# Optimization experiments

Measured on AMD Instinct MI355X. Metric: run time of the kernel, lower is better.

Reference implementation:

```python
import jax, jax.numpy as jnp
import numpy as np

EPS = 1e-6

def setup_inputs() -> dict:
    key = jax.random.key(0)
    k1, k2, k3 = jax.random.split(key, 3)
    D = 1024
    return {
        "x": jax.random.normal(k1, (2, 2048, D), dtype=jnp.float32),
        "w_norm": jnp.ones((D,), dtype=jnp.float32),
        "w_qkv": jax.random.normal(k2, (3 * D, D), dtype=jnp.float32) * (1.0 / np.sqrt(D)),
        "w_out": jax.random.normal(k3, (D, D), dtype=jnp.float32) * (1.0 / np.sqrt(D)),
        "window_size": 128,
        "n_heads": 16,
    }

def reference(x, w_norm, w_qkv, w_out, window_size, n_heads):
    B, L, D = x.shape
    H = n_heads
    dh = D // H
    skip = x
    # RMSNorm
    rms = jnp.sqrt(jnp.mean(x * x, axis=-1, keepdims=True) + EPS)
    xn = w_norm * (x / rms)
    # QKV projection (torch Linear: y = x @ W.T)
    qkv = xn @ w_qkv.T  # [B, L, 3D]
    q, k, v = jnp.split(qkv, 3, axis=-1)
    q = q.reshape(B, L, H, dh).transpose(0, 2, 1, 3)  # [B,H,L,dh]
    k = k.reshape(B, L, H, dh).transpose(0, 2, 1, 3)
    v = v.reshape(B, L, H, dh).transpose(0, 2, 1, 3)
    scores = jnp.einsum("bhid,bhjd->bhij", q, k) / np.sqrt(dh)  # [B,H,L,L]
    # Symmetric window: token i attends to j in [i - w//2, i + w//2]
    idx = jnp.arange(L)
    half = window_size // 2
    band = jnp.abs(idx[:, None] - idx[None, :]) <= half  # [L, L]
    scores = jnp.where(band, scores, -jnp.inf)
    attn = jax.nn.softmax(scores, axis=-1)  # zeros outside band, matches torch loop
    out = jnp.einsum("bhij,bhjd->bhid", attn, v)  # [B,H,L,dh]
    out = out.transpose(0, 2, 1, 3).reshape(B, L, D)
    out = out @ w_out.T
    return out + skip
```

## Files before the change

### kernel.cpp

```cpp
#include <hip/hip_runtime.h>
#include <hip/hip_bf16.h>
#include <cstdint>

typedef float f32x4 __attribute__((ext_vector_type(4)));
typedef float f32x16 __attribute__((ext_vector_type(16)));
typedef short s16x8 __attribute__((ext_vector_type(8)));
typedef short s16x4 __attribute__((ext_vector_type(4)));
typedef unsigned int u32x2 __attribute__((ext_vector_type(2)));
typedef unsigned int u32x4 __attribute__((ext_vector_type(4)));

constexpr int B_ = 2, L_ = 2048, D_ = 1024, H_ = 16, DH = 64, HALF = 64;
constexpr int M_ROWS = B_ * L_;
constexpr int QKV_N = 3 * D_;

__device__ __forceinline__ void gload16(const void* g, void* l) {
    __builtin_amdgcn_global_load_lds(
        (const __attribute__((address_space(1))) unsigned int*)g,
        (__attribute__((address_space(3))) unsigned int*)l, 16, 0, 0);
}

__device__ __forceinline__ void cfence() {
    __builtin_amdgcn_sched_barrier(0);
    asm volatile("" ::: "memory");
}

__global__ __launch_bounds__(256) void prep_kernel(const float* __restrict__ x,
                                                   const float* __restrict__ wn,
                                                   const float* __restrict__ wq,
                                                   const float* __restrict__ wo,
                                                   __hip_bfloat16* __restrict__ xn,
                                                   __hip_bfloat16* __restrict__ oq,
                                                   __hip_bfloat16* __restrict__ oo) {
    constexpr int NQ4 = QKV_N * D_ / 4;
    constexpr int NCVT = NQ4 + D_ * D_ / 4;
    constexpr int CVTBLK = NCVT / 256;
    int bid = blockIdx.x;
    if (bid < CVTBLK) {
        int i = bid * 256 + threadIdx.x;
        const float* src; __hip_bfloat16* dst; int j;
        if (i < NQ4) { src = wq; dst = oq; j = i; }
        else         { src = wo; dst = oo; j = i - NQ4; }
        float4 v = reinterpret_cast<const float4*>(src)[j];
        s16x4 pk;
        float vals[4] = {v.x, v.y, v.z, v.w};
#pragma unroll
        for (int e = 0; e < 4; ++e) {
            __hip_bfloat16 t = __float2bfloat16(vals[e]);
            pk[e] = *reinterpret_cast<short*>(&t);
        }
        *(s16x4*)(dst + (size_t)j * 4) = pk;
    } else {
        int w = threadIdx.x >> 6, lane = threadIdx.x & 63;
        int row = (bid - CVTBLK) * 4 + w;
        const float4* xr = reinterpret_cast<const float4*>(x + (size_t)row * D_);
        const float4* wr = reinterpret_cast<const float4*>(wn);
        float4 v[4];
        float ss = 0.f;
#pragma unroll
        for (int c = 0; c < 4; ++c) {
            v[c] = xr[c * 64 + lane];
            ss += v[c].x * v[c].x + v[c].y * v[c].y + v[c].z * v[c].z + v[c].w * v[c].w;
        }
#pragma unroll
        for (int off = 32; off; off >>= 1) ss += __shfl_xor(ss, off);
        float rinv = rsqrtf(ss * (1.0f / D_) + 1e-6f);
#pragma unroll
        for (int c = 0; c < 4; ++c) {
            float4 wv = wr[c * 64 + lane];
            s16x4 pk;
            float vals[4] = {v[c].x * rinv * wv.x, v[c].y * rinv * wv.y,
                             v[c].z * rinv * wv.z, v[c].w * rinv * wv.w};
#pragma unroll
            for (int e = 0; e < 4; ++e) {
                __hip_bfloat16 t = __float2bfloat16(vals[e]);
                pk[e] = *reinterpret_cast<short*>(&t);
            }
            *(s16x4*)(xn + (size_t)row * D_ + (c * 64 + lane) * 4) = pk;
        }
    }
}

__global__ __launch_bounds__(512, 2) void gemm_qkv_kernel(const __hip_bfloat16* __restrict__ A,
                                                          const __hip_bfloat16* __restrict__ Bt,
                                                          __hip_bfloat16* __restrict__ Cbf,
                                                          __hip_bfloat16* __restrict__ vT,
                                                          int M, int N, int K) {
    constexpr int ATILE = 16384;
    constexpr int BUFB = 32768;
    __shared__ __align__(16) char smem[4 * BUFB];

    const int tid = threadIdx.x;
    const int lane = tid & 63;
    const int wid = tid >> 6;

    int nwg = gridDim.x * gridDim.y;
    int lin = blockIdx.y * gridDim.x + blockIdx.x;
    int cpx = nwg >> 3;
    int swz = (lin & 7) * cpx + (lin >> 3);
    int bx = swz % gridDim.x;
    int by = swz / gridDim.x;

    const int rowBase = by * 256;
    const int colBase = bx * 256;
    const int NT = K >> 5;

    const int r0 = tid >> 2;
    const int cA = ((tid & 3) ^ ((r0 ^ (r0 >> 2)) & 3)) << 3;
    const __hip_bfloat16* aG = A + (size_t)(rowBase + r0) * K + cA;
    const __hip_bfloat16* bG = Bt + (size_t)(colBase + r0) * K + cA;
    const int dstW = wid << 10;

    const int wm = wid >> 2, wn = wid & 3;
    const int l15 = lane & 15, hi = lane >> 4;
    const int swzl = (l15 ^ (l15 >> 2)) & 3;
    const int aRd = wm * 8192 + l15 * 64 + ((hi ^ swzl) << 4);
    const int bRd = ATILE + wn * 4096 + l15 * 64 + ((hi ^ swzl) << 4);

    f32x4 acc[8][4];
#pragma unroll
    for (int m = 0; m < 8; ++m)
#pragma unroll
        for (int n = 0; n < 4; ++n) acc[m][n] = (f32x4){0.f, 0.f, 0.f, 0.f};

    auto STAGE = [&](int tt) {
        char* base = smem + (tt & 3) * BUFB + dstW;
        const __hip_bfloat16* as = aG + (size_t)tt * 32;
        const __hip_bfloat16* bs = bG + (size_t)tt * 32;
        gload16(as, base);
        gload16(as + (size_t)128 * K, base + 8192);
        gload16(bs, base + ATILE);
        gload16(bs + (size_t)128 * K, base + ATILE + 8192);
    };

    STAGE(0);
    STAGE(1);

    for (int t = 0; t < NT; ++t) {
        if (t + 2 < NT) {
            STAGE(t + 2);
            asm volatile("s_waitcnt vmcnt(8)" ::: "memory");
        } else if (t + 1 < NT) {
            asm volatile("s_waitcnt vmcnt(4)" ::: "memory");
        } else {
            asm volatile("s_waitcnt vmcnt(0)" ::: "memory");
        }
        asm volatile("s_waitcnt lgkmcnt(0)" ::: "memory");
        __builtin_amdgcn_s_barrier();
        cfence();

        const char* tb = smem + (t & 3) * BUFB;
        s16x8 af[8], bf[4];
#pragma unroll
        for (int mf = 0; mf < 8; ++mf)
            af[mf] = *(const s16x8*)(tb + aRd + mf * 1024);
#pragma unroll
        for (int nf = 0; nf < 4; ++nf)
            bf[nf] = *(const s16x8*)(tb + bRd + nf * 1024);

        __builtin_amdgcn_s_setprio(1);
#pragma unroll
        for (int mf = 0; mf < 8; ++mf)
#pragma unroll
            for (int nf = 0; nf < 4; ++nf)
                acc[mf][nf] = __builtin_amdgcn_mfma_f32_16x16x32_bf16(af[mf], bf[nf],
                                                                      acc[mf][nf], 0, 0, 0);
        __builtin_amdgcn_s_setprio(0);
    }

    if (colBase < 2 * D_) {
#pragma unroll
        for (int mf = 0; mf < 8; ++mf)
#pragma unroll
            for (int nf = 0; nf < 4; ++nf) {
                int col = colBase + wn * 64 + nf * 16 + l15;
                int row0 = rowBase + wm * 128 + mf * 16 + 4 * hi;
#pragma unroll
                for (int r = 0; r < 4; ++r)
                    Cbf[(size_t)(row0 + r) * N + col] = __float2bfloat16(acc[mf][nf][r]);
            }
    } else {
        int bb2 = rowBase >> 11, i0 = rowBase & (L_ - 1);
#pragma unroll
        for (int p = 0; p < 2; ++p) {
            if (p) __syncthreads();
            if ((wn >> 1) == p) {
#pragma unroll
                for (int mf = 0; mf < 8; ++mf)
#pragma unroll
                    for (int nf = 0; nf < 4; ++nf) {
                        int clp = (wn & 1) * 64 + nf * 16 + l15;
#pragma unroll
                        for (int r = 0; r < 4; ++r) {
                            int rl = wm * 128 + mf * 16 + 4 * hi + r;
                            __hip_bfloat16 t = __float2bfloat16(acc[mf][nf][r]);
                            *(short*)(smem + clp * 528 + rl * 2) = *reinterpret_cast<short*>(&t);
                        }
                    }
            }
            __syncthreads();
            {
                int c = tid >> 2, qd = tid & 3;
                int gcol = colBase + p * 128 + c - 2 * D_;
                int hh = gcol >> 6, dd = gcol & 63;
                __hip_bfloat16* dstp = vT + ((size_t)(bb2 * H_ + hh) * DH + dd) * L_ + i0 + qd * 64;
#pragma unroll
                for (int ch = 0; ch < 8; ++ch)
                    *(s16x8*)(dstp + ch * 8) = *(const s16x8*)(smem + c * 528 + qd * 128 + ch * 16);
            }
        }
    }
}

__global__ __launch_bounds__(256, 3) void gemm_proj_kernel(const __hip_bfloat16* __restrict__ A,
                                                           const __hip_bfloat16* __restrict__ Bt,
                                                           float* __restrict__ Cf,
                                                           const float* __restrict__ resid,
                                                           int M, int N, int K) {
    constexpr int BM = 128, BN = 64;
    constexpr int ATILE = BM * 64;
    constexpr int BTILE = BN * 64;
    constexpr int BUFB = ATILE + BTILE;
    __shared__ __align__(16) char smem[4 * BUFB];

    const int tid = threadIdx.x;
    const int lane = tid & 63;
    const int wid = tid >> 6;

    int nwg = gridDim.x * gridDim.y;
    int lin = blockIdx.y * gridDim.x + blockIdx.x;
    int cpx = nwg >> 3;
    int swz = (lin & 7) * cpx + (lin >> 3);
    int bx = swz % gridDim.x;
    int by = swz / gridDim.x;

    const int rowBase = by * BM;
    const int colBase = bx * BN;
    const int NT = K >> 5;

    const int r0 = tid >> 2;
    const int cS = ((tid & 3) ^ ((r0 ^ (r0 >> 2)) & 3)) << 3;
    const __hip_bfloat16* aG = A + (size_t)(rowBase + r0) * K + cS;
    const __hip_bfloat16* bG = Bt + (size_t)(colBase + r0) * K + cS;
    const int dstW = wid << 10;

    const int wm = wid >> 1, wn = wid & 1;
    const int l15 = lane & 15, hi = lane >> 4;
    const int swzl = (l15 ^ (l15 >> 2)) & 3;
    const int aRd = wm * 4096 + l15 * 64 + ((hi ^ swzl) << 4);
    const int bRd = ATILE + wn * 2048 + l15 * 64 + ((hi ^ swzl) << 4);

    f32x4 acc[4][2];
#pragma unroll
    for (int m = 0; m < 4; ++m)
#pragma unroll
        for (int n = 0; n < 2; ++n) acc[m][n] = (f32x4){0.f, 0.f, 0.f, 0.f};

    auto STAGE = [&](int tt) {
        char* base = smem + (tt & 3) * BUFB + dstW;
        const __hip_bfloat16* as = aG + (size_t)tt * 32;
        const __hip_bfloat16* bs = bG + (size_t)tt * 32;
        gload16(as, base);
        gload16(as + (size_t)64 * K, base + 4096);
        gload16(bs, base + ATILE);
    };

    STAGE(0);
    STAGE(1);

    for (int t = 0; t < NT; ++t) {
        if (t + 2 < NT) {
            STAGE(t + 2);
            asm volatile("s_waitcnt vmcnt(6)" ::: "memory");
        } else if (t + 1 < NT) {
            asm volatile("s_waitcnt vmcnt(3)" ::: "memory");
        } else {
            asm volatile("s_waitcnt vmcnt(0)" ::: "memory");
        }
        asm volatile("s_waitcnt lgkmcnt(0)" ::: "memory");
        __builtin_amdgcn_s_barrier();
        cfence();

        const char* tb = smem + (t & 3) * BUFB;
        s16x8 af[4], bf[2];
#pragma unroll
        for (int mf = 0; mf < 4; ++mf)
            af[mf] = *(const s16x8*)(tb + aRd + mf * 1024);
#pragma unroll
        for (int nf = 0; nf < 2; ++nf)
            bf[nf] = *(const s16x8*)(tb + bRd + nf * 1024);

        __builtin_amdgcn_s_setprio(1);
#pragma unroll
        for (int mf = 0; mf < 4; ++mf)
#pragma unroll
            for (int nf = 0; nf < 2; ++nf)
                acc[mf][nf] = __builtin_amdgcn_mfma_f32_16x16x32_bf16(af[mf], bf[nf],
                                                                      acc[mf][nf], 0, 0, 0);
        __builtin_amdgcn_s_setprio(0);
    }

#pragma unroll
    for (int mf = 0; mf < 4; ++mf)
#pragma unroll
        for (int nf = 0; nf < 2; ++nf) {
            int col = colBase + wn * 32 + nf * 16 + l15;
            int row0 = rowBase + wm * 64 + mf * 16 + 4 * hi;
#pragma unroll
            for (int r = 0; r < 4; ++r)
                Cf[(size_t)(row0 + r) * N + col] = acc[mf][nf][r] + resid[(size_t)(row0 + r) * N + col];
        }
}

__global__ __launch_bounds__(128, 2) void attn_mfma_kernel(const __hip_bfloat16* __restrict__ qkv,
                                                           const __hip_bfloat16* __restrict__ vT,
                                                           __hip_bfloat16* __restrict__ attn) {
    int tid = threadIdx.x;
    int w = tid >> 6;
    int lane = tid & 63;
    int l31 = lane & 31, hi1 = lane >> 5;
    int tq = blockIdx.x, h = blockIdx.y, b = blockIdx.z;
    int qbase = tq * 64 + 32 * w;
    int kb = qbase - HALF;
    int qg = qbase + l31;
    const __hip_bfloat16* qkvb = qkv + (size_t)(b * L_) * QKV_N;
    const __hip_bfloat16* vTg = vT + (size_t)(b * H_ + h) * DH * L_;

    s16x8 qf[4];
#pragma unroll
    for (int kk = 0; kk < 4; ++kk)
        qf[kk] = *(const s16x8*)(qkvb + (size_t)qg * QKV_N + h * DH + kk * 16 + hi1 * 8);

    f32x16 T[5];
#pragma unroll
    for (int kt = 0; kt < 5; ++kt) T[kt] = (f32x16)(0.f);
#pragma unroll
    for (int kt = 0; kt < 5; ++kt) {
        int keyg = kb + 32 * kt + l31;
        int kc = keyg < 0 ? 0 : (keyg > L_ - 1 ? L_ - 1 : keyg);
        const __hip_bfloat16* kp = qkvb + (size_t)kc * QKV_N + D_ + h * DH + hi1 * 8;
#pragma unroll
        for (int kk = 0; kk < 4; ++kk) {
            s16x8 kf = *(const s16x8*)(kp + kk * 16);
            T[kt] = __builtin_amdgcn_mfma_f32_32x32x16_bf16(kf, qf[kk], T[kt], 0, 0, 0);
        }
    }

    float mx = -1e30f;
#pragma unroll
    for (int kt = 0; kt < 5; ++kt) {
#pragma unroll
        for (int r = 0; r < 16; ++r) {
            int koff = (r & 3) + 8 * (r >> 2) + 4 * hi1;
            int keyg = kb + 32 * kt + koff;
            int del = keyg - qg;
            bool ok = (del >= -HALF) && (del <= HALF) && (keyg >= 0) && (keyg < L_);
            float t = ok ? T[kt][r] * 0.125f : -1e30f;
            T[kt][r] = t;
            mx = fmaxf(mx, t);
        }
    }
    mx = fmaxf(mx, __shfl_xor(mx, 32));
    float sum = 0.f;
#pragma unroll
    for (int kt = 0; kt < 5; ++kt) {
#pragma unroll
        for (int r = 0; r < 16; ++r) {
            float p = __expf(T[kt][r] - mx);
            T[kt][r] = p;
            sum += p;
        }
    }
    sum += __shfl_xor(sum, 32);
    float inv = 1.0f / sum;

    u32x4 pu[10];
#pragma unroll
    for (int kt = 0; kt < 5; ++kt) {
#pragma unroll
        for (int s = 0; s < 2; ++s) {
            unsigned P0, P1, P2, P3;
            asm("v_cvt_pk_bf16_f32 %0, %1, %2" : "=v"(P0) : "v"(T[kt][8 * s + 0]), "v"(T[kt][8 * s + 1]));
            asm("v_cvt_pk_bf16_f32 %0, %1, %2" : "=v"(P1) : "v"(T[kt][8 * s + 2]), "v"(T[kt][8 * s + 3]));
            asm("v_cvt_pk_bf16_f32 %0, %1, %2" : "=v"(P2) : "v"(T[kt][8 * s + 4]), "v"(T[kt][8 * s + 5]));
            asm("v_cvt_pk_bf16_f32 %0, %1, %2" : "=v"(P3) : "v"(T[kt][8 * s + 6]), "v"(T[kt][8 * s + 7]));
            u32x2 sA = __builtin_amdgcn_permlane32_swap(P0, P2, false, false);
            u32x2 sB = __builtin_amdgcn_permlane32_swap(P1, P3, false, false);
            pu[2 * kt + s] = (u32x4){sA[0], sB[0], sA[1], sB[1]};
        }
    }

    f32x16 O[2];
#pragma unroll
    for (int dt = 0; dt < 2; ++dt) O[dt] = (f32x16)(0.f);
#pragma unroll
    for (int t = 0; t < 10; ++t) {
        int kv = kb + 16 * t + 8 * hi1;
        kv = kv < 0 ? 0 : (kv > L_ - 8 ? L_ - 8 : kv);
        s16x8 pf = __builtin_bit_cast(s16x8, pu[t]);
#pragma unroll
        for (int dt = 0; dt < 2; ++dt) {
            s16x8 vf = *(const s16x8*)(vTg + (size_t)(32 * dt + l31) * L_ + kv);
            O[dt] = __builtin_amdgcn_mfma_f32_32x32x16_bf16(vf, pf, O[dt], 0, 0, 0);
        }
    }

    __hip_bfloat16* ob = attn + (size_t)(b * L_ + qg) * D_ + h * DH;
#pragma unroll
    for (int dt = 0; dt < 2; ++dt) {
#pragma unroll
        for (int rr = 0; rr < 4; ++rr) {
            s16x4 pk4;
#pragma unroll
            for (int j = 0; j < 4; ++j) {
                __hip_bfloat16 tb = __float2bfloat16(O[dt][4 * rr + j] * inv);
                pk4[j] = *reinterpret_cast<short*>(&tb);
            }
            *(s16x4*)(ob + 32 * dt + 8 * rr + 4 * hi1) = pk4;
        }
    }
}

extern "C" void kernel_launch(void* const* d_in, const int* in_sizes, int n_in,
                              void* d_out, int out_size, void* d_ws, size_t ws_size,
                              hipStream_t stream) {
    const float* x      = (const float*)d_in[0];
    const float* w_norm = (const float*)d_in[1];
    const float* w_qkv  = (const float*)d_in[2];
    const float* w_out  = (const float*)d_in[3];

    char* ws = (char*)d_ws;
    __hip_bfloat16* xn   = (__hip_bfloat16*)(ws);
    __hip_bfloat16* wq   = (__hip_bfloat16*)(ws + (8u  << 20));
    __hip_bfloat16* wo   = (__hip_bfloat16*)(ws + (14u << 20));
    __hip_bfloat16* qkv  = (__hip_bfloat16*)(ws + (16u << 20));
    __hip_bfloat16* attn = (__hip_bfloat16*)(ws + (40u << 20));
    __hip_bfloat16* vT   = (__hip_bfloat16*)(ws + (48u << 20));
    float* out = (float*)d_out;

    prep_kernel<<<4096 + M_ROWS / 4, 256, 0, stream>>>(x, w_norm, w_qkv, w_out, xn, wq, wo);

    gemm_qkv_kernel<<<dim3(QKV_N / 256, M_ROWS / 256), 512, 0, stream>>>(
        xn, wq, qkv, vT, M_ROWS, QKV_N, D_);

    attn_mfma_kernel<<<dim3(L_ / 64, H_, B_), 128, 0, stream>>>(qkv, vT, attn);

    gemm_proj_kernel<<<dim3(D_ / 64, M_ROWS / 128), 256, 0, stream>>>(
        attn, wo, out, x, M_ROWS, D_, D_);
}
```

Measured before the change: 89.91 us.

## Deepen QKV GEMM pipeline with register double-buffered A fragments

Restructures the QKV GEMM main loop to prefetch three stages ahead and to load the next tile's A fragments into a second register set while the current MFMAs run. The loop is unrolled by two so the register buffers swap without copies, and NT is made a compile-time constant. The V-transpose epilogue gains a barrier before reusing shared memory and packs four bf16 values into one 8-byte LDS store. This costs more VGPRs, which could cause spills at the 512-thread, two-block launch bound, and NT is hardcoded to K=1024.

```diff
diff --git a/kernel.cpp b/kernel.cpp
--- a/kernel.cpp
+++ b/kernel.cpp
@@ -87,6 +87,7 @@
                                                           int M, int N, int K) {
     constexpr int ATILE = 16384;
     constexpr int BUFB = 32768;
+    constexpr int NT = 32;
     __shared__ __align__(16) char smem[4 * BUFB];
 
     const int tid = threadIdx.x;
@@ -102,7 +103,6 @@
 
     const int rowBase = by * 256;
     const int colBase = bx * 256;
-    const int NT = K >> 5;
 
     const int r0 = tid >> 2;
     const int cA = ((tid & 3) ^ ((r0 ^ (r0 >> 2)) & 3)) << 3;
@@ -134,37 +134,47 @@
 
     STAGE(0);
     STAGE(1);
-
-    for (int t = 0; t < NT; ++t) {
-        if (t + 2 < NT) {
-            STAGE(t + 2);
-            asm volatile("s_waitcnt vmcnt(8)" ::: "memory");
-        } else if (t + 1 < NT) {
-            asm volatile("s_waitcnt vmcnt(4)" ::: "memory");
-        } else {
-            asm volatile("s_waitcnt vmcnt(0)" ::: "memory");
-        }
-        asm volatile("s_waitcnt lgkmcnt(0)" ::: "memory");
-        __builtin_amdgcn_s_barrier();
-        cfence();
-
+    STAGE(2);
+    asm volatile("s_waitcnt vmcnt(4)\n\ts_barrier" ::: "memory");
+    cfence();
+
+    s16x8 aA[8], aB[8], bc[4];
+#pragma unroll
+    for (int mf = 0; mf < 8; ++mf)
+        aA[mf] = *(const s16x8*)(smem + aRd + mf * 1024);
+
+    auto body = [&](int t, s16x8 (&cur)[8], s16x8 (&nxt)[8]) {
+        if (t + 1 < NT) {
+            if (t + 2 < NT)
+                asm volatile("s_waitcnt vmcnt(4)\n\ts_barrier" ::: "memory");
+            else
+                asm volatile("s_waitcnt vmcnt(0)\n\ts_barrier" ::: "memory");
+            cfence();
+        }
+        if (t + 3 < NT) STAGE(t + 3);
         const char* tb = smem + (t & 3) * BUFB;
-        s16x8 af[8], bf[4];
+#pragma unroll
+        for (int nf = 0; nf < 4; ++nf)
+            bc[nf] = *(const s16x8*)(tb + bRd + nf * 1024);
+        if (t + 1 < NT) {
+            const char* nb = smem + ((t + 1) & 3) * BUFB;
+#pragma unroll
+            for (int mf = 0; mf < 8; ++mf)
+                nxt[mf] = *(const s16x8*)(nb + aRd + mf * 1024);
+        }
+        __builtin_amdgcn_s_setprio(1);
 #pragma unroll
         for (int mf = 0; mf < 8; ++mf)
-            af[mf] = *(const s16x8*)(tb + aRd + mf * 1024);
-#pragma unroll
-        for (int nf = 0; nf < 4; ++nf)
-            bf[nf] = *(const s16x8*)(tb + bRd + nf * 1024);
-
-        __builtin_amdgcn_s_setprio(1);
-#pragma unroll
-        for (int mf = 0; mf < 8; ++mf)
 #pragma unroll
             for (int nf = 0; nf < 4; ++nf)
-                acc[mf][nf] = __builtin_amdgcn_mfma_f32_16x16x32_bf16(af[mf], bf[nf],
+                acc[mf][nf] = __builtin_amdgcn_mfma_f32_16x16x32_bf16(cur[mf], bc[nf],
                                                                       acc[mf][nf], 0, 0, 0);
         __builtin_amdgcn_s_setprio(0);
+    };
+
+    for (int tt = 0; tt < NT; tt += 2) {
+        body(tt, aA, aB);
+        body(tt + 1, aB, aA);
     }
 
     if (colBase < 2 * D_) {
@@ -179,6 +189,7 @@
                     Cbf[(size_t)(row0 + r) * N + col] = __float2bfloat16(acc[mf][nf][r]);
             }
     } else {
+        __syncthreads();
         int bb2 = rowBase >> 11, i0 = rowBase & (L_ - 1);
 #pragma unroll
         for (int p = 0; p < 2; ++p) {
@@ -189,12 +200,14 @@
 #pragma unroll
                     for (int nf = 0; nf < 4; ++nf) {
                         int clp = (wn & 1) * 64 + nf * 16 + l15;
+                        int rlb = wm * 128 + mf * 16 + 4 * hi;
+                        s16x4 pk;
 #pragma unroll
                         for (int r = 0; r < 4; ++r) {
-                            int rl = wm * 128 + mf * 16 + 4 * hi + r;
                             __hip_bfloat16 t = __float2bfloat16(acc[mf][nf][r]);
-                            *(short*)(smem + clp * 528 + rl * 2) = *reinterpret_cast<short*>(&t);
+                            pk[r] = *reinterpret_cast<short*>(&t);
                         }
+                        *(s16x4*)(smem + clp * 528 + rlb * 2) = pk;
                     }
             }
             __syncthreads();
```

New measurement: 91.31 us. No clear change (+1.5%).

## Restructure QKV GEMM into BK=64 double-buffered, four-phase interleaved load/MFMA schedule

Applied to the files above, without the earlier changes.

Changes the QKV GEMM main loop from a 4-deep ring of K=32 tiles to a double buffer of K=64 tiles with an XOR-swizzled 128-byte-row layout. Each iteration is split into four phases that alternate LDS fragment reads, staged prefetch of the next tile's quarters, and MFMA sub-blocks, with barriers between phases. The intent is to overlap global-to-LDS traffic with compute and halve the loop-iteration count. The V-transpose epilogue now packs four bf16 values into one 8-byte LDS store. The cost is many more barriers per iteration, a hardcoded NT=16 that assumes K=1024, and the full 128 KB of LDS per block, which may limit occupancy.

```diff
diff --git a/kernel.cpp b/kernel.cpp
--- a/kernel.cpp
+++ b/kernel.cpp
@@ -22,6 +22,12 @@
 __device__ __forceinline__ void cfence() {
     __builtin_amdgcn_sched_barrier(0);
     asm volatile("" ::: "memory");
+}
+
+__device__ __forceinline__ void phasebar() {
+    cfence();
+    __builtin_amdgcn_s_barrier();
+    cfence();
 }
 
 __global__ __launch_bounds__(256) void prep_kernel(const float* __restrict__ x,
@@ -85,9 +91,10 @@
                                                           __hip_bfloat16* __restrict__ Cbf,
                                                           __hip_bfloat16* __restrict__ vT,
                                                           int M, int N, int K) {
-    constexpr int ATILE = 16384;
-    constexpr int BUFB = 32768;
-    __shared__ __align__(16) char smem[4 * BUFB];
+    constexpr int AREG = 32768;
+    constexpr int BUFB = 65536;
+    constexpr int NT = 16;
+    __shared__ __align__(16) char smem[2 * BUFB];
 
     const int tid = threadIdx.x;
     const int lane = tid & 63;
@@ -102,19 +109,9 @@
 
     const int rowBase = by * 256;
     const int colBase = bx * 256;
-    const int NT = K >> 5;
-
-    const int r0 = tid >> 2;
-    const int cA = ((tid & 3) ^ ((r0 ^ (r0 >> 2)) & 3)) << 3;
-    const __hip_bfloat16* aG = A + (size_t)(rowBase + r0) * K + cA;
-    const __hip_bfloat16* bG = Bt + (size_t)(colBase + r0) * K + cA;
-    const int dstW = wid << 10;
 
     const int wm = wid >> 2, wn = wid & 3;
     const int l15 = lane & 15, hi = lane >> 4;
-    const int swzl = (l15 ^ (l15 >> 2)) & 3;
-    const int aRd = wm * 8192 + l15 * 64 + ((hi ^ swzl) << 4);
-    const int bRd = ATILE + wn * 4096 + l15 * 64 + ((hi ^ swzl) << 4);
 
     f32x4 acc[8][4];
 #pragma unroll
@@ -122,49 +119,81 @@
 #pragma unroll
         for (int n = 0; n < 4; ++n) acc[m][n] = (f32x4){0.f, 0.f, 0.f, 0.f};
 
-    auto STAGE = [&](int tt) {
-        char* base = smem + (tt & 3) * BUFB + dstW;
-        const __hip_bfloat16* as = aG + (size_t)tt * 32;
-        const __hip_bfloat16* bs = bG + (size_t)tt * 32;
-        gload16(as, base);
-        gload16(as + (size_t)128 * K, base + 8192);
-        gload16(bs, base + ATILE);
-        gload16(bs + (size_t)128 * K, base + ATILE + 8192);
+    auto STG = [&](int tt, int hs) {
+        char* dst = smem + (tt & 1) * BUFB + hs * 16384 + (wid << 10);
+#pragma unroll
+        for (int j = 0; j < 2; ++j) {
+            int o = j * 8192 + (wid << 10) + lane * 16;
+            int row = o >> 7;
+            int ch = ((o >> 4) & 7) ^ (row & 7);
+            const __hip_bfloat16* src = (hs < 2)
+                ? A + (size_t)(rowBase + hs * 128 + row) * K + tt * 64 + ch * 8
+                : Bt + (size_t)(colBase + (hs - 2) * 128 + row) * K + tt * 64 + ch * 8;
+            gload16(src, dst + j * 8192);
+        }
     };
-
-    STAGE(0);
-    STAGE(1);
-
+    auto LDA = [&](s16x8* fa, const char* buf, int mh) {
+#pragma unroll
+        for (int mf = 0; mf < 4; ++mf)
+#pragma unroll
+            for (int kk = 0; kk < 2; ++kk) {
+                int r = wm * 128 + mh * 64 + mf * 16 + l15;
+                int ch = kk * 4 + hi;
+                fa[mf * 2 + kk] = *(const s16x8*)(buf + r * 128 + ((ch ^ (r & 7)) << 4));
+            }
+    };
+    auto LDB = [&](s16x8* fb, const char* buf, int nh) {
+#pragma unroll
+        for (int nf = 0; nf < 2; ++nf)
+#pragma unroll
+            for (int kk = 0; kk < 2; ++kk) {
+                int r = wn * 64 + nh * 32 + nf * 16 + l15;
+                int ch = kk * 4 + hi;
+                fb[nf * 2 + kk] = *(const s16x8*)(buf + AREG + r * 128 + ((ch ^ (r & 7)) << 4));
+            }
+    };
+    auto MMA = [&](const s16x8* fa, const s16x8* fb, int mh, int nh) {
+        __builtin_amdgcn_s_setprio(1);
+#pragma unroll
+        for (int kk = 0; kk < 2; ++kk)
+#pragma unroll
+            for (int mf = 0; mf < 4; ++mf)
+#pragma unroll
+                for (int nf = 0; nf < 2; ++nf)
+                    acc[mh * 4 + mf][nh * 2 + nf] = __builtin_amdgcn_mfma_f32_16x16x32_bf16(
+                        fa[mf * 2 + kk], fb[nf * 2 + kk], acc[mh * 4 + mf][nh * 2 + nf], 0, 0, 0);
+        __builtin_amdgcn_s_setprio(0);
+    };
+
+    STG(0, 0); STG(0, 1); STG(0, 2); STG(0, 3);
+    asm volatile("s_waitcnt vmcnt(0)" ::: "memory");
+    __builtin_amdgcn_s_barrier();
+    cfence();
+
+    s16x8 fa[8], fb0[4], fb1[4];
     for (int t = 0; t < NT; ++t) {
-        if (t + 2 < NT) {
-            STAGE(t + 2);
-            asm volatile("s_waitcnt vmcnt(8)" ::: "memory");
-        } else if (t + 1 < NT) {
-            asm volatile("s_waitcnt vmcnt(4)" ::: "memory");
-        } else {
-            asm volatile("s_waitcnt vmcnt(0)" ::: "memory");
-        }
-        asm volatile("s_waitcnt lgkmcnt(0)" ::: "memory");
-        __builtin_amdgcn_s_barrier();
-        cfence();
-
-        const char* tb = smem + (t & 3) * BUFB;
-        s16x8 af[8], bf[4];
-#pragma unroll
-        for (int mf = 0; mf < 8; ++mf)
-            af[mf] = *(const s16x8*)(tb + aRd + mf * 1024);
-#pragma unroll
-        for (int nf = 0; nf < 4; ++nf)
-            bf[nf] = *(const s16x8*)(tb + bRd + nf * 1024);
-
-        __builtin_amdgcn_s_setprio(1);
-#pragma unroll
-        for (int mf = 0; mf < 8; ++mf)
-#pragma unroll
-            for (int nf = 0; nf < 4; ++nf)
-                acc[mf][nf] = __builtin_amdgcn_mfma_f32_16x16x32_bf16(af[mf], bf[nf],
-                                                                      acc[mf][nf], 0, 0, 0);
-        __builtin_amdgcn_s_setprio(0);
+        const char* buf = smem + (t & 1) * BUFB;
+        const bool pf = (t + 1 < NT);
+        LDA(fa, buf, 0); LDB(fb0, buf, 0);
+        if (pf) STG(t + 1, 0);
+        phasebar();
+        MMA(fa, fb0, 0, 0);
+        phasebar();
+        LDB(fb1, buf, 1);
+        if (pf) STG(t + 1, 1);
+        phasebar();
+        MMA(fa, fb1, 0, 1);
+        phasebar();
+        LDA(fa, buf, 1);
+        if (pf) STG(t + 1, 2);
+        phasebar();
+        MMA(fa, fb0, 1, 0);
+        phasebar();
+        if (pf) STG(t + 1, 3);
+        phasebar();
+        MMA(fa, fb1, 1, 1);
+        asm volatile("s_waitcnt vmcnt(0)" ::: "memory");
+        phasebar();
     }
 
     if (colBase < 2 * D_) {
@@ -179,6 +208,7 @@
                     Cbf[(size_t)(row0 + r) * N + col] = __float2bfloat16(acc[mf][nf][r]);
             }
     } else {
+        __syncthreads();
         int bb2 = rowBase >> 11, i0 = rowBase & (L_ - 1);
 #pragma unroll
         for (int p = 0; p < 2; ++p) {
@@ -189,12 +219,14 @@
 #pragma unroll
                     for (int nf = 0; nf < 4; ++nf) {
                         int clp = (wn & 1) * 64 + nf * 16 + l15;
+                        int rlb = wm * 128 + mf * 16 + 4 * hi;
+                        s16x4 pk;
 #pragma unroll
                         for (int r = 0; r < 4; ++r) {
-                            int rl = wm * 128 + mf * 16 + 4 * hi + r;
                             __hip_bfloat16 t = __float2bfloat16(acc[mf][nf][r]);
-                            *(short*)(smem + clp * 528 + rl * 2) = *reinterpret_cast<short*>(&t);
+                            pk[r] = *reinterpret_cast<short*>(&t);
                         }
+                        *(s16x4*)(smem + clp * 528 + rlb * 2) = pk;
                     }
             }
             __syncthreads();
```

Result: no change. 89.68 us (-0.3%).

## Interleave QKV GEMM loads with MFMA quarters using new LDS swizzle

Applied to the files above, without the earlier changes.

Restructures the QKV GEMM main loop so each K-step is split into four MFMA quarters. The global-to-LDS prefetch loads for step t+2 are spread between the quarters, with barriers in between, and fragment reads are partially overlapped with MFMA work. It also changes the LDS layout and XOR swizzle to pack two rows per 128-byte line, hardcodes the K-step count, and packs the V-transpose epilogue stores into 8-byte writes. The added barriers per iteration could cost more than the finer-grained overlap gains, and the hardcoded NT assumes K=1024.

```diff
diff --git a/kernel.cpp b/kernel.cpp
--- a/kernel.cpp
+++ b/kernel.cpp
@@ -85,8 +85,9 @@
                                                           __hip_bfloat16* __restrict__ Cbf,
                                                           __hip_bfloat16* __restrict__ vT,
                                                           int M, int N, int K) {
-    constexpr int ATILE = 16384;
+    constexpr int BOFF = 16384;
     constexpr int BUFB = 32768;
+    constexpr int NT = 32;
     __shared__ __align__(16) char smem[4 * BUFB];
 
     const int tid = threadIdx.x;
@@ -102,19 +103,22 @@
 
     const int rowBase = by * 256;
     const int colBase = bx * 256;
-    const int NT = K >> 5;
-
-    const int r0 = tid >> 2;
-    const int cA = ((tid & 3) ^ ((r0 ^ (r0 >> 2)) & 3)) << 3;
-    const __hip_bfloat16* aG = A + (size_t)(rowBase + r0) * K + cA;
-    const __hip_bfloat16* bG = Bt + (size_t)(colBase + r0) * K + cA;
+
+    const int sR = tid >> 3;
+    const int su = (tid & 7) ^ (sR & 7);
+    const int sMrow = 2 * sR + (su >> 2);
+    const int sCol = (su & 3) * 8;
+    const __hip_bfloat16* aG0 = A + (size_t)(rowBase + sMrow) * K + sCol;
+    const __hip_bfloat16* aG1 = A + (size_t)(rowBase + 128 + sMrow) * K + sCol;
+    const __hip_bfloat16* bG0 = Bt + (size_t)(colBase + sMrow) * K + sCol;
+    const __hip_bfloat16* bG1 = Bt + (size_t)(colBase + 128 + sMrow) * K + sCol;
     const int dstW = wid << 10;
 
     const int wm = wid >> 2, wn = wid & 3;
     const int l15 = lane & 15, hi = lane >> 4;
-    const int swzl = (l15 ^ (l15 >> 2)) & 3;
-    const int aRd = wm * 8192 + l15 * 64 + ((hi ^ swzl) << 4);
-    const int bRd = ATILE + wn * 4096 + l15 * 64 + ((hi ^ swzl) << 4);
+    const int sRd = (((l15 & 1) << 2) | hi) ^ ((l15 >> 1) & 7);
+    const int aRdB = (wm * 64 + (l15 >> 1)) * 128 + sRd * 16;
+    const int bRdB = BOFF + (wn * 32 + (l15 >> 1)) * 128 + sRd * 16;
 
     f32x4 acc[8][4];
 #pragma unroll
@@ -122,49 +126,56 @@
 #pragma unroll
         for (int n = 0; n < 4; ++n) acc[m][n] = (f32x4){0.f, 0.f, 0.f, 0.f};
 
-    auto STAGE = [&](int tt) {
-        char* base = smem + (tt & 3) * BUFB + dstW;
-        const __hip_bfloat16* as = aG + (size_t)tt * 32;
-        const __hip_bfloat16* bs = bG + (size_t)tt * 32;
-        gload16(as, base);
-        gload16(as + (size_t)128 * K, base + 8192);
-        gload16(bs, base + ATILE);
-        gload16(bs + (size_t)128 * K, base + ATILE + 8192);
+    auto STG = [&](int tt, int u) {
+        char* dst = smem + (tt & 3) * BUFB + ((u & 2) ? BOFF : 0) + ((u & 1) << 13) + dstW;
+        const __hip_bfloat16* src = (u == 0) ? aG0 : (u == 1) ? aG1 : (u == 2) ? bG0 : bG1;
+        gload16(src + (size_t)tt * 32, dst);
     };
-
-    STAGE(0);
-    STAGE(1);
-
+    auto LDA = [&](s16x8* fa, const char* buf, int mh) {
+#pragma unroll
+        for (int mf = 0; mf < 4; ++mf)
+            fa[mf] = *(const s16x8*)(buf + aRdB + mh * 4096 + mf * 1024);
+    };
+    auto LDB = [&](s16x8* fb, const char* buf, int nh) {
+#pragma unroll
+        for (int nf = 0; nf < 2; ++nf)
+            fb[nf] = *(const s16x8*)(buf + bRdB + nh * 2048 + nf * 1024);
+    };
+    auto MMA = [&](const s16x8* fa, const s16x8* fb, int mh, int nh) {
+        __builtin_amdgcn_s_setprio(1);
+#pragma unroll
+        for (int mf = 0; mf < 4; ++mf)
+#pragma unroll
+            for (int nf = 0; nf < 2; ++nf)
+                acc[mh * 4 + mf][nh * 2 + nf] = __builtin_amdgcn_mfma_f32_16x16x32_bf16(
+                    fa[mf], fb[nf], acc[mh * 4 + mf][nh * 2 + nf], 0, 0, 0);
+        __builtin_amdgcn_s_setprio(0);
+    };
+
+    STG(0, 0); STG(0, 1); STG(0, 2); STG(0, 3);
+    STG(1, 0); STG(1, 1); STG(1, 2); STG(1, 3);
+
+    s16x8 fa0[4], fa1[4], fb0[2], fb1[2];
     for (int t = 0; t < NT; ++t) {
-        if (t + 2 < NT) {
-            STAGE(t + 2);
-            asm volatile("s_waitcnt vmcnt(8)" ::: "memory");
-        } else if (t + 1 < NT) {
-            asm volatile("s_waitcnt vmcnt(4)" ::: "memory");
-        } else {
-            asm volatile("s_waitcnt vmcnt(0)" ::: "memory");
-        }
-        asm volatile("s_waitcnt lgkmcnt(0)" ::: "memory");
-        __builtin_amdgcn_s_barrier();
+        const char* buf = smem + (t & 3) * BUFB;
+        const bool pf = (t + 2 < NT);
+        if (pf) STG(t + 2, 0);
+        if (pf)                asm volatile("s_waitcnt vmcnt(5)\n\ts_barrier" ::: "memory");
+        else if (t + 1 < NT)   asm volatile("s_waitcnt vmcnt(4)\n\ts_barrier" ::: "memory");
+        else                   asm volatile("s_waitcnt vmcnt(0)\n\ts_barrier" ::: "memory");
         cfence();
-
-        const char* tb = smem + (t & 3) * BUFB;
-        s16x8 af[8], bf[4];
-#pragma unroll
-        for (int mf = 0; mf < 8; ++mf)
-            af[mf] = *(const s16x8*)(tb + aRd + mf * 1024);
-#pragma unroll
-        for (int nf = 0; nf < 4; ++nf)
-            bf[nf] = *(const s16x8*)(tb + bRd + nf * 1024);
-
-        __builtin_amdgcn_s_setprio(1);
-#pragma unroll
-        for (int mf = 0; mf < 8; ++mf)
-#pragma unroll
-            for (int nf = 0; nf < 4; ++nf)
-                acc[mf][nf] = __builtin_amdgcn_mfma_f32_16x16x32_bf16(af[mf], bf[nf],
-                                                                      acc[mf][nf], 0, 0, 0);
-        __builtin_amdgcn_s_setprio(0);
+        LDA(fa0, buf, 0); LDB(fb0, buf, 0); LDB(fb1, buf, 1);
+        MMA(fa0, fb0, 0, 0);
+        if (pf) STG(t + 2, 1);
+        cfence(); __builtin_amdgcn_s_barrier(); cfence();
+        LDA(fa1, buf, 1);
+        MMA(fa0, fb1, 0, 1);
+        if (pf) STG(t + 2, 2);
+        cfence(); __builtin_amdgcn_s_barrier(); cfence();
+        MMA(fa1, fb0, 1, 0);
+        if (pf) STG(t + 2, 3);
+        cfence(); __builtin_amdgcn_s_barrier(); cfence();
+        MMA(fa1, fb1, 1, 1);
     }
 
     if (colBase < 2 * D_) {
@@ -179,6 +190,7 @@
                     Cbf[(size_t)(row0 + r) * N + col] = __float2bfloat16(acc[mf][nf][r]);
             }
     } else {
+        __syncthreads();
         int bb2 = rowBase >> 11, i0 = rowBase & (L_ - 1);
 #pragma unroll
         for (int p = 0; p < 2; ++p) {
@@ -189,12 +201,14 @@
 #pragma unroll
                     for (int nf = 0; nf < 4; ++nf) {
                         int clp = (wn & 1) * 64 + nf * 16 + l15;
+                        int rlb = wm * 128 + mf * 16 + 4 * hi;
+                        s16x4 pk;
 #pragma unroll
                         for (int r = 0; r < 4; ++r) {
-                            int rl = wm * 128 + mf * 16 + 4 * hi + r;
                             __hip_bfloat16 t = __float2bfloat16(acc[mf][nf][r]);
-                            *(short*)(smem + clp * 528 + rl * 2) = *reinterpret_cast<short*>(&t);
+                            pk[r] = *reinterpret_cast<short*>(&t);
                         }
+                        *(s16x4*)(smem + clp * 528 + rlb * 2) = pk;
                     }
             }
             __syncthreads();
```

Result: faster. 86.67 us (-3.6%).
